# Performance work log

Measured on AMD Instinct MI355X. Metric: run time of the kernel, lower is better.

The kernel has to match this reference:

```python
import jax, jax.numpy as jnp
import numpy as np

TEMP = 0.1


def setup_inputs() -> dict:
    key = jax.random.key(0)
    k1, k2 = jax.random.split(key)
    B, Q, D, K = 4, 4096, 512, 8192
    h = jax.random.normal(k1, (B, Q, D), dtype=jnp.float32)
    codebook = jax.random.normal(k2, (K, D), dtype=jnp.float32)
    return {"h": h, "codebook": codebook}


def reference(h, codebook):
    # Squared L2 distances via the matmul expansion trick:
    # ||h - e||^2 = ||h||^2 - 2 h.e + ||e||^2  -> same math as
    # (h.unsqueeze(2) - codebook).pow(2).sum(-1), without the (B,Q,K,D) blowup.
    h_sq = jnp.sum(h * h, axis=-1, keepdims=True)            # (B, Q, 1)
    e_sq = jnp.sum(codebook * codebook, axis=-1)             # (K,)
    cross = jnp.einsum('bqd,kd->bqk', h, codebook)           # (B, Q, K)
    distances = h_sq - 2.0 * cross + e_sq                    # (B, Q, K)
    q_k = jax.nn.softmax(-distances / TEMP, axis=-1)         # (B, Q, K)
    z_e = jnp.einsum('bqk,kd->bqd', q_k, codebook)           # (B, Q, D)
    # Straight-through estimator: forward value is z_e, gradient is identity w.r.t. h.
    z_q = h + jax.lax.stop_gradient(z_e - h)
    return z_q
```

## Files before the change

### kernel.cpp

```cpp
#include <hip/hip_runtime.h>


typedef short  bf16x8 __attribute__((ext_vector_type(8)));
typedef float  f32x4  __attribute__((ext_vector_type(4)));

#define BQ      256
#define KC      64
#define DD      512
#define NCODES  8192
#define NQUART  4
#define QCODES  (NCODES / NQUART)
#define NCHUNK  (QCODES / KC)
#define CAP     16
#define TH2     52.0f
#define PRUNE   40.0f

#define SC_CROSS 28.853900817779268f
#define SC_ESQ   14.426950408889634f

static __device__ __forceinline__ unsigned short f2bf(float x) {
    unsigned int u = __float_as_uint(x);
    u += 0x7fffu + ((u >> 16) & 1u);
    return (unsigned short)(u >> 16);
}

static __device__ __forceinline__ void gload_lds16(const void* g, void* l) {
    __builtin_amdgcn_global_load_lds(
        (const __attribute__((address_space(1))) unsigned int*)g,
        (__attribute__((address_space(3))) unsigned int*)l, 16, 0, 0);
}
static __device__ __forceinline__ void gload_lds4(const void* g, void* l) {
    __builtin_amdgcn_global_load_lds(
        (const __attribute__((address_space(1))) unsigned int*)g,
        (__attribute__((address_space(3))) unsigned int*)l, 4, 0, 0);
}

__global__ __launch_bounds__(256)
void vq_convert_kernel(const float* __restrict__ cb,
                       unsigned short* __restrict__ cbswz,
                       float* __restrict__ esq)
{
    const int w     = threadIdx.x >> 6;
    const int lane  = threadIdx.x & 63;
    const int rbase = blockIdx.x * 32 + w * 8;
#pragma unroll 1
    for (int i = 0; i < 8; ++i) {
        const int r = rbase + i;
        const float* src = cb + (size_t)r * DD + lane * 8;
        float4 a = *reinterpret_cast<const float4*>(src);
        float4 b = *reinterpret_cast<const float4*>(src + 4);
        float v[8] = {a.x, a.y, a.z, a.w, b.x, b.y, b.z, b.w};
        float s2 = 0.f;
        bf16x8 o;
#pragma unroll
        for (int j = 0; j < 8; ++j) { s2 += v[j] * v[j]; o[j] = (short)f2bf(v[j]); }
#pragma unroll
        for (int off = 32; off > 0; off >>= 1) s2 += __shfl_xor(s2, off);
        const int u = lane ^ (r & 7);
        *reinterpret_cast<bf16x8*>(cbswz + (size_t)r * DD + u * 8) = o;
        if (lane == 0) esq[r] = s2;
    }
}

__global__ __launch_bounds__(512, 2)
void vq_scan_kernel(const float* __restrict__ h,
                    const unsigned short* __restrict__ cbswz,
                    const float* __restrict__ esqg,
                    uint2* __restrict__ wlist,
                    unsigned int* __restrict__ wcnt)
{
    __shared__ __align__(16) unsigned short sC[2][KC * DD];
    __shared__ __align__(16) float sEsq[2][KC];
    __shared__ int sCnt[BQ];

    const int tid  = threadIdx.x;
    const int w    = tid >> 6;
    const int lane = tid & 63;
    const int c16  = lane & 15;
    const int ub   = lane >> 4;
    const int bid  = blockIdx.x;
    const int kq   = bid & 3;
    const int qt   = bid >> 2;
    const int qb   = qt * BQ;
    const int g0q  = kq * QCODES;

    if (tid < BQ) sCnt[tid] = 0;

    const int qrowA = qb + w * 32 + c16;
    const int dsub  = ub * 8;
    bf16x8 hfA[16], hfB[16];
#pragma unroll
    for (int k = 0; k < 16; ++k) {
        const float* sA = h + (size_t)qrowA * DD + k * 32 + dsub;
        const float* sB = sA + (size_t)16 * DD;
        float4 a0 = *reinterpret_cast<const float4*>(sA);
        float4 a1 = *reinterpret_cast<const float4*>(sA + 4);
        float4 b0 = *reinterpret_cast<const float4*>(sB);
        float4 b1 = *reinterpret_cast<const float4*>(sB + 4);
        bf16x8 fa, fb;
        fa[0]=(short)f2bf(a0.x); fa[1]=(short)f2bf(a0.y); fa[2]=(short)f2bf(a0.z); fa[3]=(short)f2bf(a0.w);
        fa[4]=(short)f2bf(a1.x); fa[5]=(short)f2bf(a1.y); fa[6]=(short)f2bf(a1.z); fa[7]=(short)f2bf(a1.w);
        fb[0]=(short)f2bf(b0.x); fb[1]=(short)f2bf(b0.y); fb[2]=(short)f2bf(b0.z); fb[3]=(short)f2bf(b0.w);
        fb[4]=(short)f2bf(b1.x); fb[5]=(short)f2bf(b1.y); fb[6]=(short)f2bf(b1.z); fb[7]=(short)f2bf(b1.w);
        hfA[k] = fa; hfB[k] = fb;
    }

    const int rowlocA = w * 32 + c16;
    const int rowlocB = rowlocA + 16;
    const size_t lbA  = ((size_t)(qb + rowlocA) * NQUART + kq) * CAP;
    const size_t lbB  = ((size_t)(qb + rowlocB) * NQUART + kq) * CAP;

    float mrunA = -1e38f, mrunB = -1e38f;

    auto stage = [&](int b, int ct) {
        const char* gc = (const char*)cbswz + ((size_t)g0q + (size_t)ct * KC) * (DD * 2);
#pragma unroll
        for (int r = 0; r < 8; ++r)
            gload_lds16(gc + r * 8192 + w * 1024 + lane * 16,
                        (char*)&sC[b][0] + r * 8192 + w * 1024);
        if (w == 0)
            gload_lds4((const char*)(esqg + g0q + ct * KC) + lane * 4,
                       (char*)&sEsq[b][0]);
    };

    auto scan_chunk = [&](int cur, int gbase, bool append) {
        const float thrA = mrunA - TH2, thrB = mrunB - TH2;
        float mlA = -1e38f, mlB = -1e38f;
#pragma unroll 1
        for (int rt = 0; rt < 4; ++rt) {
            const int crow = rt * 16 + c16;
            const int swz  = crow & 7;
            const unsigned short* cbase = &sC[cur][crow * DD];
            f32x4 aA0 = {0,0,0,0}, aA1 = {0,0,0,0}, aB0 = {0,0,0,0}, aB1 = {0,0,0,0};
#pragma unroll
            for (int k = 0; k < 16; k += 2) {
                bf16x8 a0 = *reinterpret_cast<const bf16x8*>(&cbase[(((k    ) * 4 + ub) ^ swz) * 8]);
                bf16x8 a1 = *reinterpret_cast<const bf16x8*>(&cbase[(((k + 1) * 4 + ub) ^ swz) * 8]);
                aA0 = __builtin_amdgcn_mfma_f32_16x16x32_bf16(a0, hfA[k],     aA0, 0, 0, 0);
                aB0 = __builtin_amdgcn_mfma_f32_16x16x32_bf16(a0, hfB[k],     aB0, 0, 0, 0);
                aA1 = __builtin_amdgcn_mfma_f32_16x16x32_bf16(a1, hfA[k + 1], aA1, 0, 0, 0);
                aB1 = __builtin_amdgcn_mfma_f32_16x16x32_bf16(a1, hfB[k + 1], aB1, 0, 0, 0);
            }
            const int clocal = rt * 16 + ub * 4;
            f32x4 e4 = *reinterpret_cast<const f32x4*>(&sEsq[cur][clocal]);
            float LvA[4], LvB[4];
#pragma unroll
            for (int r = 0; r < 4; ++r) {
                LvA[r] = (aA0[r] + aA1[r]) * SC_CROSS - e4[r] * SC_ESQ;
                LvB[r] = (aB0[r] + aB1[r]) * SC_CROSS - e4[r] * SC_ESQ;
            }
            mlA = fmaxf(mlA, fmaxf(fmaxf(LvA[0], LvA[1]), fmaxf(LvA[2], LvA[3])));
            mlB = fmaxf(mlB, fmaxf(fmaxf(LvB[0], LvB[1]), fmaxf(LvB[2], LvB[3])));
            if (append) {
                if (LvA[0] > thrA || LvA[1] > thrA || LvA[2] > thrA || LvA[3] > thrA) {
#pragma unroll
                    for (int r = 0; r < 4; ++r)
                        if (LvA[r] > thrA) {
                            int idx = atomicAdd(&sCnt[rowlocA], 1);
                            wlist[lbA + (idx & (CAP - 1))] =
                                make_uint2((unsigned)(gbase + clocal + r), __float_as_uint(LvA[r]));
                        }
                }
                if (LvB[0] > thrB || LvB[1] > thrB || LvB[2] > thrB || LvB[3] > thrB) {
#pragma unroll
                    for (int r = 0; r < 4; ++r)
                        if (LvB[r] > thrB) {
                            int idx = atomicAdd(&sCnt[rowlocB], 1);
                            wlist[lbB + (idx & (CAP - 1))] =
                                make_uint2((unsigned)(gbase + clocal + r), __float_as_uint(LvB[r]));
                        }
                }
            }
        }
        mlA = fmaxf(mlA, __shfl_xor(mlA, 16)); mlA = fmaxf(mlA, __shfl_xor(mlA, 32));
        mlB = fmaxf(mlB, __shfl_xor(mlB, 16)); mlB = fmaxf(mlB, __shfl_xor(mlB, 32));
        mrunA = fmaxf(mrunA, mlA);
        mrunB = fmaxf(mrunB, mlB);
    };

    stage(0, 0);
    __syncthreads();
    scan_chunk(0, g0q, false);

    int cur = 0;
    for (int t = 0; t < NCHUNK; ++t) {
        if (t + 1 < NCHUNK) stage(cur ^ 1, t + 1);
        scan_chunk(cur, g0q + t * KC, true);
        __syncthreads();
        cur ^= 1;
    }

    if (tid < BQ) wcnt[(size_t)(qb + tid) * NQUART + kq] = (unsigned)sCnt[tid];
}

__global__ __launch_bounds__(512)
void vq_merge_kernel(const float* __restrict__ h,
                     const float* __restrict__ cb,
                     const uint2* __restrict__ wlist,
                     const unsigned int* __restrict__ wcnt,
                     float* __restrict__ out)
{
    const int w    = threadIdx.x >> 6;
    const int lane = threadIdx.x & 63;
    const int qg   = blockIdx.x * 8 + w;

    const int quarter = lane >> 4;
    const int slot    = lane & 15;
    const unsigned cq = wcnt[(size_t)qg * NQUART + quarter];
    const bool valid  = slot < (int)min(cq, (unsigned)CAP);

    unsigned codev = 0;
    float L = -1e38f;
    if (valid) {
        uint2 e = wlist[((size_t)qg * NQUART + quarter) * CAP + slot];
        codev = e.x;
        L = __uint_as_float(e.y);
    }
    float M = L;
#pragma unroll
    for (int off = 1; off < 64; off <<= 1) M = fmaxf(M, __shfl_xor(M, off));

    unsigned long long mask = __ballot(valid && (L > M - PRUNE));

    float hreg[8];
    const float* hp = h + (size_t)qg * DD + lane * 8;
#pragma unroll
    for (int j = 0; j < 8; ++j) hreg[j] = hp[j];

    float Mex = -1e38f, lsum = 0.f;
    float acc[8] = {0.f,0.f,0.f,0.f,0.f,0.f,0.f,0.f};
#pragma unroll 1
    while (mask) {
        const int s = __builtin_ctzll(mask);
        mask &= mask - 1;
        const int code = __shfl((int)codev, s);
        const float* cp = cb + (size_t)code * DD + lane * 8;
        float c[8];
        float dot = 0.f, s2 = 0.f;
#pragma unroll
        for (int j = 0; j < 8; ++j) {
            c[j] = cp[j];
            dot += hreg[j] * c[j];
            s2  += c[j] * c[j];
        }
#pragma unroll
        for (int off = 32; off > 0; off >>= 1) {
            dot += __shfl_xor(dot, off);
            s2  += __shfl_xor(s2,  off);
        }
        const float Lex = dot * SC_CROSS - s2 * SC_ESQ;
        const float mn  = fmaxf(Mex, Lex);
        const float f   = exp2f(Mex - mn);
        const float wj  = exp2f(Lex - mn);
        lsum = lsum * f + wj;
#pragma unroll
        for (int j = 0; j < 8; ++j) acc[j] = acc[j] * f + wj * c[j];
        Mex = mn;
    }
    const float inv = 1.0f / lsum;
    float* op = out + (size_t)qg * DD + lane * 8;
    float4 o0 = {acc[0]*inv, acc[1]*inv, acc[2]*inv, acc[3]*inv};
    float4 o1 = {acc[4]*inv, acc[5]*inv, acc[6]*inv, acc[7]*inv};
    *reinterpret_cast<float4*>(op)     = o0;
    *reinterpret_cast<float4*>(op + 4) = o1;
}

extern "C" void kernel_launch(void* const* d_in, const int* in_sizes, int n_in,
                              void* d_out, int out_size, void* d_ws, size_t ws_size,
                              hipStream_t stream) {
    const float* h  = (const float*)d_in[0];
    const float* cb = (const float*)d_in[1];
    float* out = (float*)d_out;

    char* p = (char*)d_ws;
    unsigned short* cbswz = (unsigned short*)p;                 p += (size_t)NCODES * DD * 2;
    float*          esq   = (float*)p;                          p += (size_t)NCODES * 4;
    uint2*          wlist = (uint2*)p;                          p += (size_t)16384 * NQUART * CAP * 8;
    unsigned int*   wcnt  = (unsigned int*)p;

    vq_convert_kernel<<<dim3(NCODES / 32), dim3(256), 0, stream>>>(cb, cbswz, esq);
    vq_scan_kernel<<<dim3(256), dim3(512), 0, stream>>>(h, cbswz, esq, wlist, wcnt);
    vq_merge_kernel<<<dim3(16384 / 8), dim3(512), 0, stream>>>(h, cb, wlist, wcnt, out);
}
```

Baseline: 201.1 us.

## Split codebook into octants with smaller tiles, pack candidates, pre-convert h

Restructures the scan: the codebook is split into 8 slices per query tile of 128 rows, chunks shrink to 16 codes, and the grid becomes 1024 blocks of 256 threads. This raises parallelism and occupancy. Candidate entries are packed into 32 bits (bf16 logit plus 16-bit code), and each wave keeps a protected top-2 per row so the best codes survive list overflow. The merge dedupes those entries. A separate kernel pre-converts h to swizzled bf16 so scan blocks do not repeat the conversion. The trade-offs are coarser logit precision in the prune step, tighter thresholds, an extra launch, and more per-chunk sync overhead.

```diff
diff --git a/kernel.cpp b/kernel.cpp
--- a/kernel.cpp
+++ b/kernel.cpp
@@ -4,25 +4,36 @@
 typedef short  bf16x8 __attribute__((ext_vector_type(8)));
 typedef float  f32x4  __attribute__((ext_vector_type(4)));
 
-#define BQ      256
-#define KC      64
+#define BQ      128
+#define KC      16
 #define DD      512
 #define NCODES  8192
-#define NQUART  4
-#define QCODES  (NCODES / NQUART)
-#define NCHUNK  (QCODES / KC)
-#define CAP     16
-#define TH2     52.0f
-#define PRUNE   40.0f
+#define NOCT    8
+#define OCODES  (NCODES / NOCT)
+#define NCHUNK  (OCODES / KC)
+#define NSUB    8
+#define CAPS    16
+#define NPROT   8
+#define TH2     34.0f
+#define PRUNE   44.0f
 
 #define SC_CROSS 28.853900817779268f
 #define SC_ESQ   14.426950408889634f
+
+#define SZ_CBSWZ ((size_t)NCODES * DD * 2)
+#define SZ_ESQ   ((size_t)NCODES * 4)
+#define SZ_WLIST ((size_t)16384 * NSUB * CAPS * 4)
+#define SZ_WCNT  ((size_t)16384 * NSUB * 4)
+#define SZ_HSWZ  ((size_t)512 * 16 * 2 * 64 * 16)
 
 static __device__ __forceinline__ unsigned short f2bf(float x) {
     unsigned int u = __float_as_uint(x);
     u += 0x7fffu + ((u >> 16) & 1u);
     return (unsigned short)(u >> 16);
 }
+static __device__ __forceinline__ unsigned int packE(float L, int code) {
+    return ((unsigned int)f2bf(L) << 16) | (unsigned int)code;
+}
 
 static __device__ __forceinline__ void gload_lds16(const void* g, void* l) {
     __builtin_amdgcn_global_load_lds(
@@ -36,9 +47,9 @@
 }
 
 __global__ __launch_bounds__(256)
-void vq_convert_kernel(const float* __restrict__ cb,
-                       unsigned short* __restrict__ cbswz,
-                       float* __restrict__ esq)
+void vq_convert_cb(const float* __restrict__ cb,
+                   unsigned short* __restrict__ cbswz,
+                   float* __restrict__ esq)
 {
     const int w     = threadIdx.x >> 6;
     const int lane  = threadIdx.x & 63;
@@ -62,11 +73,39 @@
     }
 }
 
-__global__ __launch_bounds__(512, 2)
+__global__ __launch_bounds__(256)
+void vq_convert_h(const float* __restrict__ h,
+                  unsigned short* __restrict__ hswz)
+{
+    const int slice = blockIdx.x;
+    const int w     = threadIdx.x >> 6;
+    const int lane  = threadIdx.x & 63;
+#pragma unroll
+    for (int i = 0; i < 4; ++i) {
+        const int k = w * 4 + i;
+#pragma unroll
+        for (int half = 0; half < 2; ++half) {
+            const int row = slice * 32 + half * 16 + (lane & 15);
+            const int d0  = k * 32 + (lane >> 4) * 8;
+            const float* src = h + (size_t)row * DD + d0;
+            float4 a = *reinterpret_cast<const float4*>(src);
+            float4 b = *reinterpret_cast<const float4*>(src + 4);
+            bf16x8 f;
+            f[0]=(short)f2bf(a.x); f[1]=(short)f2bf(a.y); f[2]=(short)f2bf(a.z); f[3]=(short)f2bf(a.w);
+            f[4]=(short)f2bf(b.x); f[5]=(short)f2bf(b.y); f[6]=(short)f2bf(b.z); f[7]=(short)f2bf(b.w);
+            *reinterpret_cast<bf16x8*>(
+                hswz + ((((size_t)slice * 16 + k) * 2 + half) * 64 + lane) * 8) = f;
+        }
+    }
+}
+
+template <bool PRE>
+__global__ __launch_bounds__(256, 3)
 void vq_scan_kernel(const float* __restrict__ h,
                     const unsigned short* __restrict__ cbswz,
                     const float* __restrict__ esqg,
-                    uint2* __restrict__ wlist,
+                    const unsigned short* __restrict__ hswz,
+                    unsigned int* __restrict__ wlist,
                     unsigned int* __restrict__ wcnt)
 {
     __shared__ __align__(16) unsigned short sC[2][KC * DD];
@@ -79,99 +118,117 @@
     const int c16  = lane & 15;
     const int ub   = lane >> 4;
     const int bid  = blockIdx.x;
-    const int kq   = bid & 3;
-    const int qt   = bid >> 2;
+    const int oct  = bid & 7;
+    const int qt   = bid >> 3;
     const int qb   = qt * BQ;
-    const int g0q  = kq * QCODES;
-
-    if (tid < BQ) sCnt[tid] = 0;
-
-    const int qrowA = qb + w * 32 + c16;
-    const int dsub  = ub * 8;
+    const int g0   = oct * OCODES;
+    const int slice = qt * 4 + w;
+
+    if (tid < BQ) sCnt[tid] = NPROT;
+
     bf16x8 hfA[16], hfB[16];
-#pragma unroll
-    for (int k = 0; k < 16; ++k) {
-        const float* sA = h + (size_t)qrowA * DD + k * 32 + dsub;
-        const float* sB = sA + (size_t)16 * DD;
-        float4 a0 = *reinterpret_cast<const float4*>(sA);
-        float4 a1 = *reinterpret_cast<const float4*>(sA + 4);
-        float4 b0 = *reinterpret_cast<const float4*>(sB);
-        float4 b1 = *reinterpret_cast<const float4*>(sB + 4);
-        bf16x8 fa, fb;
-        fa[0]=(short)f2bf(a0.x); fa[1]=(short)f2bf(a0.y); fa[2]=(short)f2bf(a0.z); fa[3]=(short)f2bf(a0.w);
-        fa[4]=(short)f2bf(a1.x); fa[5]=(short)f2bf(a1.y); fa[6]=(short)f2bf(a1.z); fa[7]=(short)f2bf(a1.w);
-        fb[0]=(short)f2bf(b0.x); fb[1]=(short)f2bf(b0.y); fb[2]=(short)f2bf(b0.z); fb[3]=(short)f2bf(b0.w);
-        fb[4]=(short)f2bf(b1.x); fb[5]=(short)f2bf(b1.y); fb[6]=(short)f2bf(b1.z); fb[7]=(short)f2bf(b1.w);
-        hfA[k] = fa; hfB[k] = fb;
+    if (PRE) {
+        const bf16x8* hs = (const bf16x8*)hswz;
+#pragma unroll
+        for (int k = 0; k < 16; ++k) {
+            hfA[k] = hs[(((size_t)slice * 16 + k) * 2 + 0) * 64 + lane];
+            hfB[k] = hs[(((size_t)slice * 16 + k) * 2 + 1) * 64 + lane];
+        }
+    } else {
+        const int qrowA = qb + w * 32 + c16;
+        const int dsub  = ub * 8;
+#pragma unroll
+        for (int k = 0; k < 16; ++k) {
+            const float* sA = h + (size_t)qrowA * DD + k * 32 + dsub;
+            const float* sB = sA + (size_t)16 * DD;
+            float4 a0 = *reinterpret_cast<const float4*>(sA);
+            float4 a1 = *reinterpret_cast<const float4*>(sA + 4);
+            float4 b0 = *reinterpret_cast<const float4*>(sB);
+            float4 b1 = *reinterpret_cast<const float4*>(sB + 4);
+            bf16x8 fa, fb;
+            fa[0]=(short)f2bf(a0.x); fa[1]=(short)f2bf(a0.y); fa[2]=(short)f2bf(a0.z); fa[3]=(short)f2bf(a0.w);
+            fa[4]=(short)f2bf(a1.x); fa[5]=(short)f2bf(a1.y); fa[6]=(short)f2bf(a1.z); fa[7]=(short)f2bf(a1.w);
+            fb[0]=(short)f2bf(b0.x); fb[1]=(short)f2bf(b0.y); fb[2]=(short)f2bf(b0.z); fb[3]=(short)f2bf(b0.w);
+            fb[4]=(short)f2bf(b1.x); fb[5]=(short)f2bf(b1.y); fb[6]=(short)f2bf(b1.z); fb[7]=(short)f2bf(b1.w);
+            hfA[k] = fa; hfB[k] = fb;
+        }
     }
 
     const int rowlocA = w * 32 + c16;
     const int rowlocB = rowlocA + 16;
-    const size_t lbA  = ((size_t)(qb + rowlocA) * NQUART + kq) * CAP;
-    const size_t lbB  = ((size_t)(qb + rowlocB) * NQUART + kq) * CAP;
+    const size_t lbA  = ((size_t)(qb + rowlocA) * NSUB + oct) * CAPS;
+    const size_t lbB  = ((size_t)(qb + rowlocB) * NSUB + oct) * CAPS;
 
     float mrunA = -1e38f, mrunB = -1e38f;
+    float b1LA = -1e38f, b2LA = -1e38f, b1LB = -1e38f, b2LB = -1e38f;
+    int   b1CA = 0, b2CA = 0, b1CB = 0, b2CB = 0;
+
+    const int swz    = c16 & 7;
+    const int clocal = ub * 4;
 
     auto stage = [&](int b, int ct) {
-        const char* gc = (const char*)cbswz + ((size_t)g0q + (size_t)ct * KC) * (DD * 2);
-#pragma unroll
-        for (int r = 0; r < 8; ++r)
-            gload_lds16(gc + r * 8192 + w * 1024 + lane * 16,
-                        (char*)&sC[b][0] + r * 8192 + w * 1024);
-        if (w == 0)
-            gload_lds4((const char*)(esqg + g0q + ct * KC) + lane * 4,
+        const char* gc = (const char*)cbswz + ((size_t)g0 + (size_t)ct * KC) * (DD * 2);
+#pragma unroll
+        for (int r = 0; r < 4; ++r)
+            gload_lds16(gc + r * 4096 + tid * 16,
+                        (char*)&sC[b][0] + r * 4096 + tid * 16);
+        if (w == 0 && lane < KC)
+            gload_lds4((const char*)(esqg + g0 + ct * KC) + lane * 4,
                        (char*)&sEsq[b][0]);
     };
 
-    auto scan_chunk = [&](int cur, int gbase, bool append) {
+    auto scan_chunk = [&](int cur, int gbase, bool append, bool track) {
         const float thrA = mrunA - TH2, thrB = mrunB - TH2;
-        float mlA = -1e38f, mlB = -1e38f;
-#pragma unroll 1
-        for (int rt = 0; rt < 4; ++rt) {
-            const int crow = rt * 16 + c16;
-            const int swz  = crow & 7;
-            const unsigned short* cbase = &sC[cur][crow * DD];
-            f32x4 aA0 = {0,0,0,0}, aA1 = {0,0,0,0}, aB0 = {0,0,0,0}, aB1 = {0,0,0,0};
-#pragma unroll
-            for (int k = 0; k < 16; k += 2) {
-                bf16x8 a0 = *reinterpret_cast<const bf16x8*>(&cbase[(((k    ) * 4 + ub) ^ swz) * 8]);
-                bf16x8 a1 = *reinterpret_cast<const bf16x8*>(&cbase[(((k + 1) * 4 + ub) ^ swz) * 8]);
-                aA0 = __builtin_amdgcn_mfma_f32_16x16x32_bf16(a0, hfA[k],     aA0, 0, 0, 0);
-                aB0 = __builtin_amdgcn_mfma_f32_16x16x32_bf16(a0, hfB[k],     aB0, 0, 0, 0);
-                aA1 = __builtin_amdgcn_mfma_f32_16x16x32_bf16(a1, hfA[k + 1], aA1, 0, 0, 0);
-                aB1 = __builtin_amdgcn_mfma_f32_16x16x32_bf16(a1, hfB[k + 1], aB1, 0, 0, 0);
-            }
-            const int clocal = rt * 16 + ub * 4;
-            f32x4 e4 = *reinterpret_cast<const f32x4*>(&sEsq[cur][clocal]);
-            float LvA[4], LvB[4];
+        const unsigned short* cbase = &sC[cur][c16 * DD];
+        f32x4 aA0 = {0,0,0,0}, aA1 = {0,0,0,0}, aB0 = {0,0,0,0}, aB1 = {0,0,0,0};
+#pragma unroll
+        for (int k = 0; k < 16; k += 2) {
+            bf16x8 a0 = *reinterpret_cast<const bf16x8*>(&cbase[(((k    ) * 4 + ub) ^ swz) * 8]);
+            bf16x8 a1 = *reinterpret_cast<const bf16x8*>(&cbase[(((k + 1) * 4 + ub) ^ swz) * 8]);
+            aA0 = __builtin_amdgcn_mfma_f32_16x16x32_bf16(a0, hfA[k],     aA0, 0, 0, 0);
+            aB0 = __builtin_amdgcn_mfma_f32_16x16x32_bf16(a0, hfB[k],     aB0, 0, 0, 0);
+            aA1 = __builtin_amdgcn_mfma_f32_16x16x32_bf16(a1, hfA[k + 1], aA1, 0, 0, 0);
+            aB1 = __builtin_amdgcn_mfma_f32_16x16x32_bf16(a1, hfB[k + 1], aB1, 0, 0, 0);
+        }
+        f32x4 e4 = *reinterpret_cast<const f32x4*>(&sEsq[cur][clocal]);
+        float LvA[4], LvB[4];
+#pragma unroll
+        for (int r = 0; r < 4; ++r) {
+            LvA[r] = (aA0[r] + aA1[r]) * SC_CROSS - e4[r] * SC_ESQ;
+            LvB[r] = (aB0[r] + aB1[r]) * SC_CROSS - e4[r] * SC_ESQ;
+        }
+        if (track) {
 #pragma unroll
             for (int r = 0; r < 4; ++r) {
-                LvA[r] = (aA0[r] + aA1[r]) * SC_CROSS - e4[r] * SC_ESQ;
-                LvB[r] = (aB0[r] + aB1[r]) * SC_CROSS - e4[r] * SC_ESQ;
-            }
-            mlA = fmaxf(mlA, fmaxf(fmaxf(LvA[0], LvA[1]), fmaxf(LvA[2], LvA[3])));
-            mlB = fmaxf(mlB, fmaxf(fmaxf(LvB[0], LvB[1]), fmaxf(LvB[2], LvB[3])));
-            if (append) {
-                if (LvA[0] > thrA || LvA[1] > thrA || LvA[2] > thrA || LvA[3] > thrA) {
-#pragma unroll
-                    for (int r = 0; r < 4; ++r)
-                        if (LvA[r] > thrA) {
-                            int idx = atomicAdd(&sCnt[rowlocA], 1);
-                            wlist[lbA + (idx & (CAP - 1))] =
-                                make_uint2((unsigned)(gbase + clocal + r), __float_as_uint(LvA[r]));
-                        }
-                }
-                if (LvB[0] > thrB || LvB[1] > thrB || LvB[2] > thrB || LvB[3] > thrB) {
-#pragma unroll
-                    for (int r = 0; r < 4; ++r)
-                        if (LvB[r] > thrB) {
-                            int idx = atomicAdd(&sCnt[rowlocB], 1);
-                            wlist[lbB + (idx & (CAP - 1))] =
-                                make_uint2((unsigned)(gbase + clocal + r), __float_as_uint(LvB[r]));
-                        }
-                }
-            }
-        }
+                const int cd = gbase + clocal + r;
+                if (LvA[r] > b1LA)      { b2LA = b1LA; b2CA = b1CA; b1LA = LvA[r]; b1CA = cd; }
+                else if (LvA[r] > b2LA) { b2LA = LvA[r]; b2CA = cd; }
+                if (LvB[r] > b1LB)      { b2LB = b1LB; b2CB = b1CB; b1LB = LvB[r]; b1CB = cd; }
+                else if (LvB[r] > b2LB) { b2LB = LvB[r]; b2CB = cd; }
+            }
+        }
+        if (append) {
+            if (LvA[0] > thrA || LvA[1] > thrA || LvA[2] > thrA || LvA[3] > thrA) {
+#pragma unroll
+                for (int r = 0; r < 4; ++r)
+                    if (LvA[r] > thrA) {
+                        int idx  = atomicAdd(&sCnt[rowlocA], 1);
+                        int slot = idx < CAPS ? idx : NPROT + ((idx - NPROT) & (NPROT - 1));
+                        wlist[lbA + slot] = packE(LvA[r], gbase + clocal + r);
+                    }
+            }
+            if (LvB[0] > thrB || LvB[1] > thrB || LvB[2] > thrB || LvB[3] > thrB) {
+#pragma unroll
+                for (int r = 0; r < 4; ++r)
+                    if (LvB[r] > thrB) {
+                        int idx  = atomicAdd(&sCnt[rowlocB], 1);
+                        int slot = idx < CAPS ? idx : NPROT + ((idx - NPROT) & (NPROT - 1));
+                        wlist[lbB + slot] = packE(LvB[r], gbase + clocal + r);
+                    }
+            }
+        }
+        float mlA = fmaxf(fmaxf(LvA[0], LvA[1]), fmaxf(LvA[2], LvA[3]));
+        float mlB = fmaxf(fmaxf(LvB[0], LvB[1]), fmaxf(LvB[2], LvB[3]));
         mlA = fmaxf(mlA, __shfl_xor(mlA, 16)); mlA = fmaxf(mlA, __shfl_xor(mlA, 32));
         mlB = fmaxf(mlB, __shfl_xor(mlB, 16)); mlB = fmaxf(mlB, __shfl_xor(mlB, 32));
         mrunA = fmaxf(mrunA, mlA);
@@ -180,23 +237,28 @@
 
     stage(0, 0);
     __syncthreads();
-    scan_chunk(0, g0q, false);
+    scan_chunk(0, g0, false, false);
 
     int cur = 0;
     for (int t = 0; t < NCHUNK; ++t) {
         if (t + 1 < NCHUNK) stage(cur ^ 1, t + 1);
-        scan_chunk(cur, g0q + t * KC, true);
+        scan_chunk(cur, g0 + t * KC, true, true);
         __syncthreads();
         cur ^= 1;
     }
 
-    if (tid < BQ) wcnt[(size_t)(qb + tid) * NQUART + kq] = (unsigned)sCnt[tid];
+    wlist[lbA + ub * 2]     = packE(b1LA, b1CA);
+    wlist[lbA + ub * 2 + 1] = packE(b2LA, b2CA);
+    wlist[lbB + ub * 2]     = packE(b1LB, b1CB);
+    wlist[lbB + ub * 2 + 1] = packE(b2LB, b2CB);
+
+    if (tid < BQ) wcnt[(size_t)(qb + tid) * NSUB + oct] = (unsigned)sCnt[tid];
 }
 
 __global__ __launch_bounds__(512)
 void vq_merge_kernel(const float* __restrict__ h,
                      const float* __restrict__ cb,
-                     const uint2* __restrict__ wlist,
+                     const unsigned int* __restrict__ wlist,
                      const unsigned int* __restrict__ wcnt,
                      float* __restrict__ out)
 {
@@ -204,23 +266,41 @@
     const int lane = threadIdx.x & 63;
     const int qg   = blockIdx.x * 8 + w;
 
-    const int quarter = lane >> 4;
-    const int slot    = lane & 15;
-    const unsigned cq = wcnt[(size_t)qg * NQUART + quarter];
-    const bool valid  = slot < (int)min(cq, (unsigned)CAP);
-
-    unsigned codev = 0;
-    float L = -1e38f;
-    if (valid) {
-        uint2 e = wlist[((size_t)qg * NQUART + quarter) * CAP + slot];
-        codev = e.x;
-        L = __uint_as_float(e.y);
-    }
-    float M = L;
-#pragma unroll
-    for (int off = 1; off < 64; off <<= 1) M = fmaxf(M, __shfl_xor(M, off));
-
-    unsigned long long mask = __ballot(valid && (L > M - PRUNE));
+    const int sl = lane >> 3;
+    const int s0 = (lane & 7) * 2;
+    const size_t base = ((size_t)qg * NSUB + sl) * CAPS;
+    const unsigned cnt   = wcnt[(size_t)qg * NSUB + sl];
+    const unsigned limit = cnt < (unsigned)CAPS ? cnt : (unsigned)CAPS;
+
+    uint2 e2 = *reinterpret_cast<const uint2*>(&wlist[base + s0]);
+    int   code0 = e2.x & 0xFFFF, code1 = e2.y & 0xFFFF;
+    float L0 = __uint_as_float(e2.x & 0xFFFF0000u);
+    float L1 = __uint_as_float(e2.y & 0xFFFF0000u);
+    bool v0 = (unsigned)s0 < limit;
+    bool v1 = (unsigned)(s0 + 1) < limit;
+
+    {
+        uint4 p0 = *reinterpret_cast<const uint4*>(&wlist[base]);
+        uint4 p1 = *reinterpret_cast<const uint4*>(&wlist[base + 4]);
+        const unsigned pc[8] = {p0.x & 0xFFFFu, p0.y & 0xFFFFu, p0.z & 0xFFFFu, p0.w & 0xFFFFu,
+                                p1.x & 0xFFFFu, p1.y & 0xFFFFu, p1.z & 0xFFFFu, p1.w & 0xFFFFu};
+        const int lim0 = (s0 >= NPROT) ? 8 : s0;
+        bool d0 = false, d1 = false;
+#pragma unroll
+        for (int j = 0; j < 8; ++j) {
+            d0 |= (j < lim0) && ((unsigned)code0 == pc[j]);
+            d1 |= (j < lim0) && ((unsigned)code1 == pc[j]);
+        }
+        d1 |= (code1 == code0) && (s0 < NPROT);
+        v0 &= !d0; v1 &= !d1;
+    }
+
+    float m = fmaxf(v0 ? L0 : -1e38f, v1 ? L1 : -1e38f);
+#pragma unroll
+    for (int off = 1; off < 64; off <<= 1) m = fmaxf(m, __shfl_xor(m, off));
+    const float thr = m - PRUNE;
+    unsigned long long mask0 = __ballot(v0 && L0 > thr);
+    unsigned long long mask1 = __ballot(v1 && L1 > thr);
 
     float hreg[8];
     const float* hp = h + (size_t)qg * DD + lane * 8;
@@ -229,34 +309,40 @@
 
     float Mex = -1e38f, lsum = 0.f;
     float acc[8] = {0.f,0.f,0.f,0.f,0.f,0.f,0.f,0.f};
+
+    auto process = [&](unsigned long long mask, int codev) {
 #pragma unroll 1
-    while (mask) {
-        const int s = __builtin_ctzll(mask);
-        mask &= mask - 1;
-        const int code = __shfl((int)codev, s);
-        const float* cp = cb + (size_t)code * DD + lane * 8;
-        float c[8];
-        float dot = 0.f, s2 = 0.f;
-#pragma unroll
-        for (int j = 0; j < 8; ++j) {
-            c[j] = cp[j];
-            dot += hreg[j] * c[j];
-            s2  += c[j] * c[j];
-        }
-#pragma unroll
-        for (int off = 32; off > 0; off >>= 1) {
-            dot += __shfl_xor(dot, off);
-            s2  += __shfl_xor(s2,  off);
-        }
-        const float Lex = dot * SC_CROSS - s2 * SC_ESQ;
-        const float mn  = fmaxf(Mex, Lex);
-        const float f   = exp2f(Mex - mn);
-        const float wj  = exp2f(Lex - mn);
-        lsum = lsum * f + wj;
-#pragma unroll
-        for (int j = 0; j < 8; ++j) acc[j] = acc[j] * f + wj * c[j];
-        Mex = mn;
-    }
+        while (mask) {
+            const int s = __builtin_ctzll(mask);
+            mask &= mask - 1;
+            const int code = __shfl(codev, s);
+            const float* cp = cb + (size_t)code * DD + lane * 8;
+            float c[8];
+            float dot = 0.f, s2 = 0.f;
+#pragma unroll
+            for (int j = 0; j < 8; ++j) {
+                c[j] = cp[j];
+                dot += hreg[j] * c[j];
+                s2  += c[j] * c[j];
+            }
+#pragma unroll
+            for (int off = 32; off > 0; off >>= 1) {
+                dot += __shfl_xor(dot, off);
+                s2  += __shfl_xor(s2,  off);
+            }
+            const float Lex = dot * SC_CROSS - s2 * SC_ESQ;
+            const float mn  = fmaxf(Mex, Lex);
+            const float f   = exp2f(Mex - mn);
+            const float wj  = exp2f(Lex - mn);
+            lsum = lsum * f + wj;
+#pragma unroll
+            for (int j = 0; j < 8; ++j) acc[j] = acc[j] * f + wj * c[j];
+            Mex = mn;
+        }
+    };
+    process(mask0, code0);
+    process(mask1, code1);
+
     const float inv = 1.0f / lsum;
     float* op = out + (size_t)qg * DD + lane * 8;
     float4 o0 = {acc[0]*inv, acc[1]*inv, acc[2]*inv, acc[3]*inv};
@@ -273,12 +359,23 @@
     float* out = (float*)d_out;
 
     char* p = (char*)d_ws;
-    unsigned short* cbswz = (unsigned short*)p;                 p += (size_t)NCODES * DD * 2;
-    float*          esq   = (float*)p;                          p += (size_t)NCODES * 4;
-    uint2*          wlist = (uint2*)p;                          p += (size_t)16384 * NQUART * CAP * 8;
-    unsigned int*   wcnt  = (unsigned int*)p;
-
-    vq_convert_kernel<<<dim3(NCODES / 32), dim3(256), 0, stream>>>(cb, cbswz, esq);
-    vq_scan_kernel<<<dim3(256), dim3(512), 0, stream>>>(h, cbswz, esq, wlist, wcnt);
+    unsigned short* cbswz = (unsigned short*)p;  p += SZ_CBSWZ;
+    float*          esq   = (float*)p;           p += SZ_ESQ;
+    unsigned int*   wlist = (unsigned int*)p;    p += SZ_WLIST;
+    unsigned int*   wcnt  = (unsigned int*)p;    p += SZ_WCNT;
+    unsigned short* hswz  = (unsigned short*)p;
+
+    const size_t need_full = SZ_CBSWZ + SZ_ESQ + SZ_WLIST + SZ_WCNT + SZ_HSWZ;
+    const bool pre = ws_size >= need_full;
+
+    vq_convert_cb<<<dim3(NCODES / 32), dim3(256), 0, stream>>>(cb, cbswz, esq);
+    if (pre) {
+        vq_convert_h<<<dim3(512), dim3(256), 0, stream>>>(h, hswz);
+        vq_scan_kernel<true><<<dim3(1024), dim3(256), 0, stream>>>(
+            h, cbswz, esq, hswz, wlist, wcnt);
+    } else {
+        vq_scan_kernel<false><<<dim3(1024), dim3(256), 0, stream>>>(
+            h, cbswz, esq, nullptr, wlist, wcnt);
+    }
     vq_merge_kernel<<<dim3(16384 / 8), dim3(512), 0, stream>>>(h, cb, wlist, wcnt, out);
 }
```

Measured after the change: 694.9 us. 246% more time.
